# Performance work log

Hardware: AMD Instinct MI355X
Metric: run time of the kernel (lower is better)

Reference implementation:

```python
import jax, jax.numpy as jnp
import numpy as np

# LLaMA-7B style BitNet b1.58 MLP dims
B, S = 2, 2048
H, I = 4096, 11008
EPS = 1e-8
QMAX = 127.0  # int8 activation range


def _ternary_weight(key, shape):
    """BitNet b1.58 absmean weight quantization: per-tensor scale, ternary {-1,0,1}."""
    w = jax.random.normal(key, shape, jnp.float32) * 0.02
    ws = jnp.mean(jnp.abs(w)) + EPS
    qw = jnp.clip(jnp.round(w / ws), -1.0, 1.0)
    return qw, ws


def setup_inputs() -> dict:
    key = jax.random.key(0)
    k0, k1, k2, k3 = jax.random.split(key, 4)
    # x arrives already absmean-quantized to int8 values (stored as float) + scalar scale
    xf = jax.random.normal(k0, (B, S, H), jnp.float32)
    xs = jnp.mean(jnp.abs(xf)) + EPS
    x = jnp.clip(jnp.round(xf / xs), -QMAX - 1, QMAX)
    qw_gate, ws_gate = _ternary_weight(k1, (I, H))
    qw_up, ws_up = _ternary_weight(k2, (I, H))
    qw_down, ws_down = _ternary_weight(k3, (H, I))
    return {"x": x, "x_scale": xs,
            "qw_gate": qw_gate, "ws_gate": ws_gate,
            "qw_up": qw_up, "ws_up": ws_up,
            "qw_down": qw_down, "ws_down": ws_down}


def absmean_quantize(x):
    """Per-tensor absmean quantization to int8 range with straight-through rounding."""
    scale = jnp.mean(jnp.abs(x)) + EPS
    c = x / scale
    q = c + jax.lax.stop_gradient(jnp.clip(jnp.round(c), -QMAX - 1, QMAX) - c)
    return q, scale


def quantized_linear(xq, xs, qw, ws):
    # integer-valued GEMM; output scale is product of input and weight scales
    out = jnp.einsum('bsh,ih->bsi', xq, qw)
    return out, xs * ws


def reference(x, x_scale, qw_gate, ws_gate, qw_up, ws_up, qw_down, ws_down):
    gate, gate_s = quantized_linear(x, x_scale, qw_gate, ws_gate)      # [B,S,I]
    up, up_s = quantized_linear(x, x_scale, qw_up, ws_up)              # [B,S,I]
    # quantized_act: dequant -> SiLU -> re-quantize (absmean)
    ga_q, ga_s = absmean_quantize(jax.nn.silu(gate * gate_s))
    # quantized elementwise matmul: multiply q-values, multiply scales, re-quantize
    inter_q, inter_s = absmean_quantize(ga_q * up * (ga_s * up_s))
    # down projection (I -> H): einsum over intermediate dim
    out = jnp.einsum('bsi,hi->bsh', inter_q, qw_down)
    return out, inter_s * ws_down
```

## Files before the change

kernel.cpp:

```cpp
#include <hip/hip_runtime.h>
#include <math.h>

#define TOK 4096
#define HD  4096
#define ID  11008

typedef int i32x4 __attribute__((ext_vector_type(4)));
typedef float f32x4v __attribute__((ext_vector_type(4)));
typedef char i8x4v __attribute__((ext_vector_type(4)));

#define GLDS16(g, l) __builtin_amdgcn_global_load_lds( \
    (const __attribute__((address_space(1))) void*)(g), \
    (__attribute__((address_space(3))) void*)(l), 16, 0, 0)

__global__ void conv_all(const float* __restrict__ x,  char* __restrict__ xq,
                         const float* __restrict__ wg, char* __restrict__ wgq,
                         const float* __restrict__ wu, char* __restrict__ wuq,
                         const float* __restrict__ wd, char* __restrict__ wdq)
{
  const long NX = (long)TOK * HD / 4, NW = (long)ID * HD / 4;
  const long total = NX + 3 * NW;
  const long stride = (long)gridDim.x * blockDim.x;
  for (long i = (long)blockIdx.x * blockDim.x + threadIdx.x; i < total;
       i += stride) {
    const f32x4v* src; i8x4v* dst; long j;
    if (i < NX)               { src = (const f32x4v*)x;  dst = (i8x4v*)xq;  j = i; }
    else if (i < NX + NW)     { src = (const f32x4v*)wg; dst = (i8x4v*)wgq; j = i - NX; }
    else if (i < NX + 2 * NW) { src = (const f32x4v*)wu; dst = (i8x4v*)wuq; j = i - NX - NW; }
    else                      { src = (const f32x4v*)wd; dst = (i8x4v*)wdq; j = i - NX - 2 * NW; }
    f32x4v v = __builtin_nontemporal_load(&src[j]);
    i8x4v o;
    o.x = (char)(int)rintf(v.x);
    o.y = (char)(int)rintf(v.y);
    o.z = (char)(int)rintf(v.z);
    o.w = (char)(int)rintf(v.w);
    dst[j] = o;
  }
}

template<int MODE>
__global__ __launch_bounds__(256, 3)
void gemm_i8(const char* __restrict__ A,
             const char* __restrict__ Bm,
             int M, int N, int K,
             float* __restrict__ Cout,
             const float* __restrict__ ga_in,
             const float* __restrict__ sc0,
             const float* __restrict__ sc1,
             double* __restrict__ sums,
             long long NN)
{
  __shared__ char As[16384];
  __shared__ char Bs[16384];
  __shared__ double red[4];

  const int tid  = threadIdx.x;
  const int w    = tid >> 6;
  const int lane = tid & 63;
  const int wr   = lane & 15;
  const int qd   = lane >> 4;
  const int wm   = (w >> 1) << 6;
  const int wn   = (w & 1) << 6;

  const int L   = blockIdx.y * gridDim.x + blockIdx.x;
  const int xcd = L & 7;
  const int r   = L >> 3;
  const int m0  = (xcd + ((r & 3) << 3)) << 7;
  const int n0  = (r >> 2) << 7;

  i32x4 acc[4][4] = {};

  const int rowL = tid >> 3;
  const int chk  = (tid & 7) ^ (rowL & 7);
  const char* gA = A  + (size_t)(m0 + rowL) * K + (chk << 4);
  const char* gB = Bm + (size_t)(n0 + rowL) * K + (chk << 4);
  const size_t rk32 = (size_t)32 * K;
  char* lA = As + (w << 10);
  char* lB = Bs + (w << 10);

  const int s7    = wr & 7;
  const int abase = ((wm + wr) << 7) + ((qd ^ s7) << 4);
  const int bbase = ((wn + wr) << 7) + ((qd ^ s7) << 4);

  for (int k0 = 0; k0 < K; k0 += 128) {
    GLDS16(gA + k0,            lA);
    GLDS16(gA + k0 +     rk32, lA + 4096);
    GLDS16(gA + k0 + 2 * rk32, lA + 8192);
    GLDS16(gA + k0 + 3 * rk32, lA + 12288);
    GLDS16(gB + k0,            lB);
    GLDS16(gB + k0 +     rk32, lB + 4096);
    GLDS16(gB + k0 + 2 * rk32, lB + 8192);
    GLDS16(gB + k0 + 3 * rk32, lB + 12288);
    __syncthreads();

#pragma unroll
    for (int h = 0; h < 2; h++) {
      const int hx = h << 6;
      i32x4 af[4], bfr[4];
#pragma unroll
      for (int i = 0; i < 4; i++)
        af[i] = *(const i32x4*)(As + ((abase + (i << 11)) ^ hx));
#pragma unroll
      for (int j = 0; j < 4; j++)
        bfr[j] = *(const i32x4*)(Bs + ((bbase + (j << 11)) ^ hx));

#pragma unroll
      for (int i = 0; i < 4; i++)
#pragma unroll
        for (int j = 0; j < 4; j++)
          acc[i][j] = __builtin_amdgcn_mfma_i32_16x16x64_i8(af[i], bfr[j],
                                                            acc[i][j], 0, 0, 0);
    }
    __syncthreads();
  }

  double lsum = 0.0;

  if (MODE == 0) {
    const float gs = sc0[0] * sc1[0];
#pragma unroll
    for (int i = 0; i < 4; i++) {
      const int mb = m0 + wm + (i << 4) + (qd << 2);
#pragma unroll
      for (int j = 0; j < 4; j++) {
        const int n = n0 + wn + (j << 4) + wr;
#pragma unroll
        for (int r2 = 0; r2 < 4; r2++) {
          float g = (float)acc[i][j][r2] * gs;
          float s = g / (1.0f + expf(-g));
          __builtin_nontemporal_store(s, &Cout[(size_t)(mb + r2) * N + n]);
          lsum += (double)fabsf(s);
        }
      }
    }
  } else if (MODE == 1) {
    const float up_s  = sc0[0] * sc1[0];
    const float ga_s  = (float)(sums[0] / (double)NN) + 1e-8f;
    const float combo = ga_s * up_s;
#pragma unroll
    for (int i = 0; i < 4; i++) {
      const int mb = m0 + wm + (i << 4) + (qd << 2);
#pragma unroll
      for (int j = 0; j < 4; j++) {
        const int n = n0 + wn + (j << 4) + wr;
#pragma unroll
        for (int r2 = 0; r2 < 4; r2++) {
          float up = (float)acc[i][j][r2];
          float ga = __builtin_nontemporal_load(
                         &ga_in[(size_t)(mb + r2) * N + n]);
          float gq = fmaxf(-128.0f, fminf(127.0f, rintf(ga / ga_s)));
          float itv = gq * up * combo;
          __builtin_nontemporal_store(itv, &Cout[(size_t)(mb + r2) * N + n]);
          lsum += (double)fabsf(itv);
        }
      }
    }
  } else {
#pragma unroll
    for (int i = 0; i < 4; i++) {
      const int mb = m0 + wm + (i << 4) + (qd << 2);
#pragma unroll
      for (int j = 0; j < 4; j++) {
        const int n = n0 + wn + (j << 4) + wr;
#pragma unroll
        for (int r2 = 0; r2 < 4; r2++)
          __builtin_nontemporal_store((float)acc[i][j][r2],
                                      &Cout[(size_t)(mb + r2) * N + n]);
      }
    }
  }

  if (MODE != 2) {
    for (int off = 32; off; off >>= 1) lsum += __shfl_down(lsum, off, 64);
    if (lane == 0) red[w] = lsum;
    __syncthreads();
    if (tid == 0) atomicAdd(&sums[MODE], red[0] + red[1] + red[2] + red[3]);
  }
}

__global__ void quant_inter(const float* __restrict__ inter,
                            char* __restrict__ outq,
                            const double* __restrict__ sums, long long NN,
                            const float* __restrict__ wsd,
                            float* __restrict__ scalar_out, int n4)
{
  const float is = (float)(sums[1] / (double)NN) + 1e-8f;
  if (blockIdx.x == 0 && threadIdx.x == 0) scalar_out[0] = is * wsd[0];
  int stride = gridDim.x * blockDim.x;
  for (int i = blockIdx.x * blockDim.x + threadIdx.x; i < n4; i += stride) {
    f32x4v v = __builtin_nontemporal_load(&((const f32x4v*)inter)[i]);
    i8x4v o;
    o.x = (char)(int)fmaxf(-128.0f, fminf(127.0f, rintf(v.x / is)));
    o.y = (char)(int)fmaxf(-128.0f, fminf(127.0f, rintf(v.y / is)));
    o.z = (char)(int)fmaxf(-128.0f, fminf(127.0f, rintf(v.z / is)));
    o.w = (char)(int)fmaxf(-128.0f, fminf(127.0f, rintf(v.w / is)));
    ((i8x4v*)outq)[i] = o;
  }
}

extern "C" void kernel_launch(void* const* d_in, const int* in_sizes, int n_in,
                              void* d_out, int out_size, void* d_ws, size_t ws_size,
                              hipStream_t stream) {
  const float* x        = (const float*)d_in[0];
  const float* x_scale  = (const float*)d_in[1];
  const float* qw_gate  = (const float*)d_in[2];
  const float* ws_gate  = (const float*)d_in[3];
  const float* qw_up    = (const float*)d_in[4];
  const float* ws_up    = (const float*)d_in[5];
  const float* qw_down  = (const float*)d_in[6];
  const float* ws_down  = (const float*)d_in[7];
  float* out = (float*)d_out;

  char* ws = (char*)d_ws;
  double* sums = (double*)ws;
  size_t off = 256;
  char* xq     = ws + off; off += (size_t)TOK * HD;
  char* wgq    = ws + off; off += (size_t)ID * HD;
  char* wuq    = ws + off; off += (size_t)ID * HD;
  char* wdq    = ws + off; off += (size_t)HD * ID;
  char* interq = ws + off; off += (size_t)TOK * ID;
  float* ga    = (float*)(ws + off); off += (size_t)TOK * ID * 4;
  float* inter = (float*)(ws + off); off += (size_t)TOK * ID * 4;

  const long long NN = (long long)TOK * ID;

  (void)hipMemsetAsync(sums, 0, 16, stream);

  conv_all<<<8192, 256, 0, stream>>>(x, xq, qw_gate, wgq, qw_up, wuq,
                                     qw_down, wdq);

  gemm_i8<0><<<dim3(ID / 128, TOK / 128), 256, 0, stream>>>(
      xq, wgq, TOK, ID, HD, ga, nullptr, x_scale, ws_gate, sums, NN);

  gemm_i8<1><<<dim3(ID / 128, TOK / 128), 256, 0, stream>>>(
      xq, wuq, TOK, ID, HD, inter, ga, x_scale, ws_up, sums, NN);

  quant_inter<<<8192, 256, 0, stream>>>(inter, interq, sums, NN, ws_down,
                                        out + (size_t)TOK * HD, (int)(NN / 4));

  gemm_i8<2><<<dim3(HD / 128, TOK / 128), 256, 0, stream>>>(
      interq, wdq, TOK, HD, ID, out, nullptr, nullptr, nullptr, sums, NN);
}
```

Before: 1.105 ms.

## Use 256x256 tiles with 4-stage LDS pipelined int8 GEMM

Reworks the int8 GEMM into 256x256 output tiles per 512-thread block, with K step 64 and a 4-buffer, 128KB LDS ring. Global-to-LDS loads run three stages ahead, with explicit vmcnt/lgkmcnt waits, split A/B staging and setprio around the MFMA bursts. The intent is to raise arithmetic intensity per byte loaded and hide memory latency behind MFMA work. The cost is much larger LDS use and more accumulator registers, which limits occupancy, plus ordering that depends on hand-placed waits and barriers.

Measured after the change: 1.228 ms. 11.1% more time.

```diff
diff --git a/kernel.cpp b/kernel.cpp
--- a/kernel.cpp
+++ b/kernel.cpp
@@ -39,7 +39,7 @@
 }
 
 template<int MODE>
-__global__ __launch_bounds__(256, 3)
+__global__ __launch_bounds__(512, 2)
 void gemm_i8(const char* __restrict__ A,
              const char* __restrict__ Bm,
              int M, int N, int K,
@@ -50,80 +50,110 @@
              double* __restrict__ sums,
              long long NN)
 {
-  __shared__ char As[16384];
-  __shared__ char Bs[16384];
-  __shared__ double red[4];
+  __shared__ __align__(16) char Ls[131072];
 
   const int tid  = threadIdx.x;
-  const int w    = tid >> 6;
+  const int wv   = tid >> 6;
   const int lane = tid & 63;
   const int wr   = lane & 15;
   const int qd   = lane >> 4;
-  const int wm   = (w >> 1) << 6;
-  const int wn   = (w & 1) << 6;
-
-  const int L   = blockIdx.y * gridDim.x + blockIdx.x;
+
+  const int WM = (wv >> 2) << 7;
+  const int WN = (wv & 3) << 6;
+
+  const int L   = blockIdx.x;
   const int xcd = L & 7;
-  const int r   = L >> 3;
-  const int m0  = (xcd + ((r & 3) << 3)) << 7;
-  const int n0  = (r >> 2) << 7;
-
-  i32x4 acc[4][4] = {};
-
-  const int rowL = tid >> 3;
-  const int chk  = (tid & 7) ^ (rowL & 7);
-  const char* gA = A  + (size_t)(m0 + rowL) * K + (chk << 4);
-  const char* gB = Bm + (size_t)(n0 + rowL) * K + (chk << 4);
-  const size_t rk32 = (size_t)32 * K;
-  char* lA = As + (w << 10);
-  char* lB = Bs + (w << 10);
-
-  const int s7    = wr & 7;
-  const int abase = ((wm + wr) << 7) + ((qd ^ s7) << 4);
-  const int bbase = ((wn + wr) << 7) + ((qd ^ s7) << 4);
-
-  for (int k0 = 0; k0 < K; k0 += 128) {
-    GLDS16(gA + k0,            lA);
-    GLDS16(gA + k0 +     rk32, lA + 4096);
-    GLDS16(gA + k0 + 2 * rk32, lA + 8192);
-    GLDS16(gA + k0 + 3 * rk32, lA + 12288);
-    GLDS16(gB + k0,            lB);
-    GLDS16(gB + k0 +     rk32, lB + 4096);
-    GLDS16(gB + k0 + 2 * rk32, lB + 8192);
-    GLDS16(gB + k0 + 3 * rk32, lB + 12288);
-    __syncthreads();
-
-#pragma unroll
-    for (int h = 0; h < 2; h++) {
-      const int hx = h << 6;
-      i32x4 af[4], bfr[4];
-#pragma unroll
-      for (int i = 0; i < 4; i++)
-        af[i] = *(const i32x4*)(As + ((abase + (i << 11)) ^ hx));
+  const int p   = L >> 3;
+  const int m0  = (xcd + ((p & 1) << 3)) << 8;
+  const int n0  = (p >> 1) << 8;
+
+  const int srow   = (wv << 5) + (lane >> 2);
+  const int schunk = (lane & 3) ^ ((lane >> 2) & 3);
+  const char* gA = A  + (size_t)(m0 + srow) * K + (schunk << 4);
+  const char* gB = Bm + (size_t)(n0 + srow) * K + (schunk << 4);
+  const size_t r16K = (size_t)16 * K;
+  char* sA = Ls + (wv << 11);
+  char* sB = Ls + 65536 + (wv << 11);
+
+  const int rsw  = (qd ^ (wr & 3)) << 4;
+  const int aoff = ((WM + wr) << 6) + rsw;
+  const int boff = ((WN + wr) << 6) + rsw;
+
+  i32x4 acc[8][4] = {};
+  const int NT = K >> 6;
+
+#define STAGE_A(t) do { const char* g_ = gA + (size_t)((t) << 6);          \
+    char* l_ = sA + (((t) & 3) << 14);                                     \
+    GLDS16(g_, l_); GLDS16(g_ + r16K, l_ + 1024); } while (0)
+#define STAGE_B(t) do { const char* g_ = gB + (size_t)((t) << 6);          \
+    char* l_ = sB + (((t) & 3) << 14);                                     \
+    GLDS16(g_, l_); GLDS16(g_ + r16K, l_ + 1024); } while (0)
+
+  STAGE_A(0); STAGE_B(0);
+  STAGE_A(1); STAGE_B(1);
+  STAGE_A(2); STAGE_B(2);
+  asm volatile("s_waitcnt vmcnt(8)" ::: "memory");
+  __builtin_amdgcn_s_barrier();
+
+#pragma unroll 4
+  for (int t = 0; t < NT; ++t) {
+    const char* bufA = Ls + ((t & 3) << 14);
+    const char* bufB = Ls + 65536 + ((t & 3) << 14);
+
+    i32x4 af[4], bf[4];
+#pragma unroll
+    for (int i = 0; i < 4; i++)
+      af[i] = *(const i32x4*)(bufA + aoff + (i << 10));
+#pragma unroll
+    for (int j = 0; j < 4; j++)
+      bf[j] = *(const i32x4*)(bufB + boff + (j << 10));
+    if (t + 3 < NT) STAGE_A(t + 3);
+    __builtin_amdgcn_s_barrier();
+    asm volatile("s_waitcnt lgkmcnt(0)" ::: "memory");
+    __builtin_amdgcn_s_setprio(1);
+#pragma unroll
+    for (int i = 0; i < 4; i++)
 #pragma unroll
       for (int j = 0; j < 4; j++)
-        bfr[j] = *(const i32x4*)(Bs + ((bbase + (j << 11)) ^ hx));
-
-#pragma unroll
-      for (int i = 0; i < 4; i++)
-#pragma unroll
-        for (int j = 0; j < 4; j++)
-          acc[i][j] = __builtin_amdgcn_mfma_i32_16x16x64_i8(af[i], bfr[j],
-                                                            acc[i][j], 0, 0, 0);
-    }
-    __syncthreads();
-  }
+        acc[i][j] = __builtin_amdgcn_mfma_i32_16x16x64_i8(af[i], bf[j],
+                                                          acc[i][j], 0, 0, 0);
+    __builtin_amdgcn_s_setprio(0);
+    __builtin_amdgcn_s_barrier();
+
+    i32x4 a2[4];
+#pragma unroll
+    for (int i = 0; i < 4; i++)
+      a2[i] = *(const i32x4*)(bufA + aoff + ((i + 4) << 10));
+    if (t + 3 < NT) STAGE_B(t + 3);
+    __builtin_amdgcn_s_barrier();
+    asm volatile("s_waitcnt lgkmcnt(0)" ::: "memory");
+    __builtin_amdgcn_s_setprio(1);
+#pragma unroll
+    for (int i = 0; i < 4; i++)
+#pragma unroll
+      for (int j = 0; j < 4; j++)
+        acc[i + 4][j] = __builtin_amdgcn_mfma_i32_16x16x64_i8(a2[i], bf[j],
+                                                              acc[i + 4][j],
+                                                              0, 0, 0);
+    __builtin_amdgcn_s_setprio(0);
+    if (t + 3 < NT)      asm volatile("s_waitcnt vmcnt(8)" ::: "memory");
+    else if (t + 2 < NT) asm volatile("s_waitcnt vmcnt(4)" ::: "memory");
+    else if (t + 1 < NT) asm volatile("s_waitcnt vmcnt(0)" ::: "memory");
+    __builtin_amdgcn_s_barrier();
+  }
+#undef STAGE_A
+#undef STAGE_B
 
   double lsum = 0.0;
 
   if (MODE == 0) {
     const float gs = sc0[0] * sc1[0];
 #pragma unroll
-    for (int i = 0; i < 4; i++) {
-      const int mb = m0 + wm + (i << 4) + (qd << 2);
+    for (int i = 0; i < 8; i++) {
+      const int mb = m0 + WM + (i << 4) + (qd << 2);
 #pragma unroll
       for (int j = 0; j < 4; j++) {
-        const int n = n0 + wn + (j << 4) + wr;
+        const int n = n0 + WN + (j << 4) + wr;
 #pragma unroll
         for (int r2 = 0; r2 < 4; r2++) {
           float g = (float)acc[i][j][r2] * gs;
@@ -138,11 +168,11 @@
     const float ga_s  = (float)(sums[0] / (double)NN) + 1e-8f;
     const float combo = ga_s * up_s;
 #pragma unroll
-    for (int i = 0; i < 4; i++) {
-      const int mb = m0 + wm + (i << 4) + (qd << 2);
+    for (int i = 0; i < 8; i++) {
+      const int mb = m0 + WM + (i << 4) + (qd << 2);
 #pragma unroll
       for (int j = 0; j < 4; j++) {
-        const int n = n0 + wn + (j << 4) + wr;
+        const int n = n0 + WN + (j << 4) + wr;
 #pragma unroll
         for (int r2 = 0; r2 < 4; r2++) {
           float up = (float)acc[i][j][r2];
@@ -157,11 +187,11 @@
     }
   } else {
 #pragma unroll
-    for (int i = 0; i < 4; i++) {
-      const int mb = m0 + wm + (i << 4) + (qd << 2);
+    for (int i = 0; i < 8; i++) {
+      const int mb = m0 + WM + (i << 4) + (qd << 2);
 #pragma unroll
       for (int j = 0; j < 4; j++) {
-        const int n = n0 + wn + (j << 4) + wr;
+        const int n = n0 + WN + (j << 4) + wr;
 #pragma unroll
         for (int r2 = 0; r2 < 4; r2++)
           __builtin_nontemporal_store((float)acc[i][j][r2],
@@ -172,9 +202,15 @@
 
   if (MODE != 2) {
     for (int off = 32; off; off >>= 1) lsum += __shfl_down(lsum, off, 64);
-    if (lane == 0) red[w] = lsum;
+    double* red = (double*)Ls;
+    if (lane == 0) red[wv] = lsum;
     __syncthreads();
-    if (tid == 0) atomicAdd(&sums[MODE], red[0] + red[1] + red[2] + red[3]);
+    if (tid == 0) {
+      double s2 = 0.0;
+#pragma unroll
+      for (int k2 = 0; k2 < 8; k2++) s2 += red[k2];
+      atomicAdd(&sums[MODE], s2);
+    }
   }
 }
 
@@ -229,15 +265,15 @@
   conv_all<<<8192, 256, 0, stream>>>(x, xq, qw_gate, wgq, qw_up, wuq,
                                      qw_down, wdq);
 
-  gemm_i8<0><<<dim3(ID / 128, TOK / 128), 256, 0, stream>>>(
+  gemm_i8<0><<<dim3((ID / 256) * (TOK / 256)), 512, 0, stream>>>(
       xq, wgq, TOK, ID, HD, ga, nullptr, x_scale, ws_gate, sums, NN);
 
-  gemm_i8<1><<<dim3(ID / 128, TOK / 128), 256, 0, stream>>>(
+  gemm_i8<1><<<dim3((ID / 256) * (TOK / 256)), 512, 0, stream>>>(
       xq, wuq, TOK, ID, HD, inter, ga, x_scale, ws_up, sums, NN);
 
   quant_inter<<<8192, 256, 0, stream>>>(inter, interq, sums, NN, ws_down,
                                         out + (size_t)TOK * HD, (int)(NN / 4));
 
-  gemm_i8<2><<<dim3(HD / 128, TOK / 128), 256, 0, stream>>>(
+  gemm_i8<2><<<dim3((HD / 256) * (TOK / 256)), 512, 0, stream>>>(
       interq, wdq, TOK, HD, ID, out, nullptr, nullptr, nullptr, sums, NN);
 }
```
